# Optimization experiments

Measured on AMD Instinct MI355X. Metric: run time of the kernel, lower is better.

The kernel has to match this reference:

```python
import jax, jax.numpy as jnp
import numpy as np

B, S, D_MODEL, N_HEADS, D_K, D_V = 2, 2048, 1024, 16, 64, 64


def setup_inputs() -> dict:
    key = jax.random.key(0)
    k1, k2, k3, k4, k5, k6, k7 = jax.random.split(key, 7)
    scale = 1.0 / np.sqrt(D_MODEL)
    inputs = {
        "input_Q": jax.random.normal(k1, (B, S, D_MODEL), dtype=jnp.float32),
        "input_K": jax.random.normal(k2, (B, S, D_MODEL), dtype=jnp.float32),
        "input_V": jax.random.normal(k3, (B, S, D_MODEL), dtype=jnp.float32),
        # causal mask: True means position is masked out (matches masked_fill_)
        "attn_mask": jnp.broadcast_to(
            ~jnp.tril(jnp.ones((S, S), dtype=bool)), (B, S, S)
        ),
        "flag": 0,
        "W_Q": jax.random.normal(k4, (D_MODEL, N_HEADS * D_K), dtype=jnp.float32) * scale,
        "W_K": jax.random.normal(k5, (D_MODEL, N_HEADS * D_K), dtype=jnp.float32) * scale,
        "W_V": jax.random.normal(k6, (D_MODEL, N_HEADS * D_V), dtype=jnp.float32) * scale,
        "W_O": jax.random.normal(k7, (N_HEADS * D_V, D_MODEL), dtype=jnp.float32) * scale,
    }
    return inputs


def reference(input_Q, input_K, input_V, attn_mask, flag, W_Q, W_K, W_V, W_O):
    b = input_Q.shape[0]
    # project and split heads: [b, h, s, d]
    Q = (input_Q @ W_Q).reshape(b, -1, N_HEADS, D_K).transpose(0, 2, 1, 3)
    K = (input_K @ W_K).reshape(b, -1, N_HEADS, D_K).transpose(0, 2, 1, 3)
    V = (input_V @ W_V).reshape(b, -1, N_HEADS, D_V).transpose(0, 2, 1, 3)
    # scaled dot-product attention with additive large-negative masking
    scores = jnp.einsum("bhqd,bhkd->bhqk", Q, K) / np.sqrt(D_K).astype(np.float32)
    scores = jnp.where(attn_mask[:, None, :, :], jnp.float32(-1e9), scores)
    attn = jax.nn.softmax(scores, axis=-1)
    context = jnp.einsum("bhqk,bhkd->bhqd", attn, V)  # [b, h, s, d_v]
    context = context.transpose(0, 2, 1, 3).reshape(b, -1, N_HEADS * D_V)
    return context @ W_O
```

## Files before the change

### kernel.cpp

```cpp
#include <hip/hip_runtime.h>

#define DEVINL __device__ __forceinline__

typedef __attribute__((ext_vector_type(8))) short short8;
typedef __attribute__((ext_vector_type(4))) float floatx4;

constexpr int S_LEN = 2048;
constexpr int DM    = 1024;
constexpr int NHEAD = 16;
constexpr int DHEAD = 64;
constexpr int BATCH = 2;
constexpr int MROWS = BATCH * S_LEN;
constexpr float LOG2E = 1.44269504f;
constexpr float SM_C1 = 0.125f * LOG2E;
constexpr float SM_C2 = -24.0f * LOG2E;

DEVINL unsigned short f2bf(float x) {
  union { float f; unsigned u; } un; un.f = x;
  unsigned u = un.u;
  return (unsigned short)((u + 0x7fffu + ((u >> 16) & 1u)) >> 16);
}
DEVINL unsigned short f2bf_fast(float x) {
  union { float f; unsigned u; } un; un.f = x;
  return (unsigned short)((un.u + 0x8000u) >> 16);
}

__global__ __launch_bounds__(256) void conv3_kernel(const float* __restrict__ s0,
                                                    const float* __restrict__ s1,
                                                    const float* __restrict__ s2,
                                                    unsigned short* __restrict__ d0,
                                                    unsigned short* __restrict__ d1,
                                                    unsigned short* __restrict__ d2) {
  const float* s = blockIdx.y == 0 ? s0 : (blockIdx.y == 1 ? s1 : s2);
  unsigned short* d = blockIdx.y == 0 ? d0 : (blockIdx.y == 1 ? d1 : d2);
  int i = (blockIdx.x * 256 + threadIdx.x) * 4;
  float4 v = *(const float4*)(s + i);
  unsigned lo = (unsigned)f2bf(v.x) | ((unsigned)f2bf(v.y) << 16);
  unsigned hi = (unsigned)f2bf(v.z) | ((unsigned)f2bf(v.w) << 16);
  *(uint2*)(d + i) = make_uint2(lo, hi);
}

__global__ __launch_bounds__(256) void trans4_kernel(const float* __restrict__ W0,
                                                     const float* __restrict__ W1,
                                                     const float* __restrict__ W2,
                                                     const float* __restrict__ W3,
                                                     unsigned short* __restrict__ T0,
                                                     unsigned short* __restrict__ T1,
                                                     unsigned short* __restrict__ T2,
                                                     unsigned short* __restrict__ T3) {
  const float* W = blockIdx.z == 0 ? W0 : (blockIdx.z == 1 ? W1 : (blockIdx.z == 2 ? W2 : W3));
  unsigned short* Wt = blockIdx.z == 0 ? T0 : (blockIdx.z == 1 ? T1 : (blockIdx.z == 2 ? T2 : T3));
  __shared__ unsigned short tile[32][33];
  int t = threadIdx.x;
  int c = t & 31, r0 = t >> 5;
  int nB = blockIdx.x * 32, kB = blockIdx.y * 32;
  for (int i = 0; i < 4; ++i) {
    int r = r0 + i * 8;
    tile[r][c] = f2bf(W[(size_t)(kB + r) * DM + nB + c]);
  }
  __syncthreads();
  for (int i = 0; i < 4; ++i) {
    int r = r0 + i * 8;
    Wt[(size_t)(nB + r) * DM + kB + c] = tile[c][r];
  }
}

__global__ __launch_bounds__(256) void vtrans_kernel(const unsigned short* __restrict__ vp,
                                                     unsigned short* __restrict__ vt) {
  const int bh = blockIdx.x;
  const int st = blockIdx.y;
  const int b = bh >> 4, h = bh & 15;
  const int s0 = st * 64;
  const int tid = threadIdx.x;
  __shared__ alignas(16) unsigned short tile[64 * 72];
#pragma unroll
  for (int j = 0; j < 2; ++j) {
    int ch = j * 256 + tid;
    int r = ch >> 3, c8 = (ch & 7) * 8;
    *(uint4*)&tile[r * 72 + c8] =
        *(const uint4*)&vp[((size_t)(b * S_LEN + s0 + r)) * DM + h * DHEAD + c8];
  }
  __syncthreads();
#pragma unroll
  for (int j = 0; j < 2; ++j) {
    int ch = j * 256 + tid;
    int d = ch >> 3, s8 = (ch & 7) * 8;
    unsigned short w[8];
#pragma unroll
    for (int e = 0; e < 8; ++e) w[e] = tile[(s8 + e) * 72 + d];
    *(uint4*)&vt[((size_t)(bh * DHEAD + d)) * S_LEN + s0 + s8] = *(const uint4*)w;
  }
}

DEVINL void load_lds16(const unsigned short* g, unsigned short* l) {
  __builtin_amdgcn_global_load_lds((const __attribute__((address_space(1))) unsigned int*)g,
                                   (__attribute__((address_space(3))) unsigned int*)l,
                                   16, 0, 0);
}

template <int MODE>
DEVINL void gemm_body(const unsigned short* __restrict__ A,
                      const unsigned short* __restrict__ Bt,
                      void* __restrict__ Cout) {
  constexpr int K = 1024, N = 1024;
  __shared__ alignas(16) unsigned short As[128 * 32];
  __shared__ alignas(16) unsigned short Bs[128 * 32];
  const int tid  = threadIdx.x;
  const int wave = tid >> 6, lane = tid & 63;
  const int quad = lane >> 4, l16 = lane & 15;
  const int mBase = blockIdx.y * 128, nBase = blockIdx.x * 128;
  const int wm = (wave >> 1) * 64, wn = (wave & 1) * 64;
  const int sr = lane >> 2;
  const int sc = (lane & 3) * 8;
  floatx4 acc[4][4] = {};

  for (int k0 = 0; k0 < K; k0 += 32) {
    __syncthreads();
#pragma unroll
    for (int j = 0; j < 2; ++j) {
      int row = wave * 32 + j * 16 + sr;
      load_lds16(A  + (size_t)(mBase + row) * K + k0 + sc, As + (wave * 32 + j * 16) * 32);
      load_lds16(Bt + (size_t)(nBase + row) * K + k0 + sc, Bs + (wave * 32 + j * 16) * 32);
    }
    __syncthreads();
    short8 af[4], bfr[4];
#pragma unroll
    for (int mt = 0; mt < 4; ++mt) af[mt]  = *(const short8*)&As[(wm + mt * 16 + l16) * 32 + quad * 8];
#pragma unroll
    for (int nt = 0; nt < 4; ++nt) bfr[nt] = *(const short8*)&Bs[(wn + nt * 16 + l16) * 32 + quad * 8];
#pragma unroll
    for (int mt = 0; mt < 4; ++mt)
#pragma unroll
      for (int nt = 0; nt < 4; ++nt)
        acc[mt][nt] = __builtin_amdgcn_mfma_f32_16x16x32_bf16(af[mt], bfr[nt], acc[mt][nt], 0, 0, 0);
  }

#pragma unroll
  for (int mt = 0; mt < 4; ++mt)
#pragma unroll
    for (int nt = 0; nt < 4; ++nt)
#pragma unroll
      for (int r = 0; r < 4; ++r) {
        int m = mBase + wm + mt * 16 + quad * 4 + r;
        int n = nBase + wn + nt * 16 + l16;
        if (MODE == 0) ((unsigned short*)Cout)[(size_t)m * N + n] = f2bf(acc[mt][nt][r]);
        else           ((float*)Cout)[(size_t)m * N + n]          = acc[mt][nt][r];
      }
}

__global__ __launch_bounds__(256) void gemm_qkv(const unsigned short* __restrict__ A0,
                                                const unsigned short* __restrict__ A1,
                                                const unsigned short* __restrict__ A2,
                                                const unsigned short* __restrict__ B0,
                                                const unsigned short* __restrict__ B1,
                                                const unsigned short* __restrict__ B2,
                                                unsigned short* __restrict__ C0,
                                                unsigned short* __restrict__ C1,
                                                unsigned short* __restrict__ C2) {
  const int z = blockIdx.z;
  const unsigned short* A  = z == 0 ? A0 : (z == 1 ? A1 : A2);
  const unsigned short* Bt = z == 0 ? B0 : (z == 1 ? B1 : B2);
  unsigned short* C        = z == 0 ? C0 : (z == 1 ? C1 : C2);
  gemm_body<0>(A, Bt, C);
}

__global__ __launch_bounds__(256) void gemm_out(const unsigned short* __restrict__ A,
                                                const unsigned short* __restrict__ Bt,
                                                float* __restrict__ C) {
  gemm_body<1>(A, Bt, C);
}

__global__ __launch_bounds__(256) void attn_kernel(const unsigned short* __restrict__ Qp,
                                                   const unsigned short* __restrict__ Kp,
                                                   const unsigned short* __restrict__ Vtg,
                                                   unsigned short* __restrict__ ctx) {
  const int qt = gridDim.x - 1 - blockIdx.x;
  const int bh = blockIdx.y;
  const int b  = bh >> 4, h = bh & 15;
  const int tid = threadIdx.x;
  const int wave = tid >> 6, lane = tid & 63;
  const int quad = lane >> 4, l16 = lane & 15;
  const int Q0 = qt * 128;
  const int nT = 2 * qt + 2;

  __shared__ alignas(16) unsigned short Ks[64 * 72];
  __shared__ alignas(16) unsigned short Vs[64 * 72];
  __shared__ alignas(16) unsigned short Ps[4][32 * 72];

  const unsigned short* Kbh = Kp  + (size_t)(b * S_LEN) * DM + h * DHEAD;
  const unsigned short* Vbh = Vtg + (size_t)(bh * DHEAD) * S_LEN;

  const int sr = tid >> 3, sc8 = (tid & 7) * 8;
  const unsigned short* kptr = Kbh + (size_t)sr * DM + sc8;
  const unsigned short* vptr = Vbh + (size_t)sr * S_LEN + sc8;
  unsigned short* ksl = Ks + sr * 72 + sc8;
  unsigned short* vsl = Vs + sr * 72 + sc8;

  const int rowbase = Q0 + wave * 32;
  short8 qf[2][2];
#pragma unroll
  for (int mt = 0; mt < 2; ++mt) {
    const size_t qrow = ((size_t)(b * S_LEN + rowbase + mt * 16 + l16)) * DM + h * DHEAD;
    qf[mt][0] = *(const short8*)&Qp[qrow + quad * 8];
    qf[mt][1] = *(const short8*)&Qp[qrow + 32 + quad * 8];
  }

  floatx4 o[2][4] = {};
  float rs[2][4] = {};
  unsigned short* Pw = &Ps[wave][0];

  uint4 kr0 = *(const uint4*)kptr;
  uint4 kr1 = *(const uint4*)(kptr + (size_t)32 * DM);
  uint4 vr0 = *(const uint4*)vptr;
  uint4 vr1 = *(const uint4*)(vptr + (size_t)32 * S_LEN);

  for (int t = 0; t < nT; ++t) {
    const int kb = t * 64;
    __syncthreads();
    *(uint4*)ksl              = kr0;
    *(uint4*)(ksl + 32 * 72)  = kr1;
    *(uint4*)vsl              = vr0;
    *(uint4*)(vsl + 32 * 72)  = vr1;
    __syncthreads();

    {
      const int kbn = (t + 1 < nT) ? (t + 1) * 64 : 0;
      kr0 = *(const uint4*)(kptr + (size_t)kbn * DM);
      kr1 = *(const uint4*)(kptr + (size_t)(kbn + 32) * DM);
      vr0 = *(const uint4*)(vptr + kbn);
      vr1 = *(const uint4*)(vptr + (size_t)32 * S_LEN + kbn);
    }

    floatx4 sc[2][4];
#pragma unroll
    for (int nt = 0; nt < 4; ++nt) {
      short8 kf0 = *(const short8*)&Ks[(nt * 16 + l16) * 72 + quad * 8];
      short8 kf1 = *(const short8*)&Ks[(nt * 16 + l16) * 72 + 32 + quad * 8];
#pragma unroll
      for (int mt = 0; mt < 2; ++mt) {
        floatx4 a = {};
        a = __builtin_amdgcn_mfma_f32_16x16x32_bf16(qf[mt][0], kf0, a, 0, 0, 0);
        a = __builtin_amdgcn_mfma_f32_16x16x32_bf16(qf[mt][1], kf1, a, 0, 0, 0);
        sc[mt][nt] = a;
      }
    }

    const bool masked = (t >= nT - 2);
#pragma unroll
    for (int mt = 0; mt < 2; ++mt)
#pragma unroll
      for (int nt = 0; nt < 4; ++nt) {
        const int colg = kb + nt * 16 + l16;
#pragma unroll
        for (int r = 0; r < 4; ++r) {
          float p = __builtin_amdgcn_exp2f(fmaf(sc[mt][nt][r], SM_C1, SM_C2));
          if (masked && colg > rowbase + mt * 16 + quad * 4 + r) p = 0.f;
          rs[mt][r] += p;
          Pw[(mt * 16 + quad * 4 + r) * 72 + nt * 16 + l16] = f2bf_fast(p);
        }
      }

    short8 vf[4][2];
#pragma unroll
    for (int dt = 0; dt < 4; ++dt) {
      vf[dt][0] = *(const short8*)&Vs[(dt * 16 + l16) * 72 + quad * 8];
      vf[dt][1] = *(const short8*)&Vs[(dt * 16 + l16) * 72 + 32 + quad * 8];
    }
#pragma unroll
    for (int mt = 0; mt < 2; ++mt) {
      short8 pf0 = *(const short8*)&Pw[(mt * 16 + l16) * 72 + quad * 8];
      short8 pf1 = *(const short8*)&Pw[(mt * 16 + l16) * 72 + 32 + quad * 8];
#pragma unroll
      for (int dt = 0; dt < 4; ++dt) {
        o[mt][dt] = __builtin_amdgcn_mfma_f32_16x16x32_bf16(pf0, vf[dt][0], o[mt][dt], 0, 0, 0);
        o[mt][dt] = __builtin_amdgcn_mfma_f32_16x16x32_bf16(pf1, vf[dt][1], o[mt][dt], 0, 0, 0);
      }
    }
  }

#pragma unroll
  for (int mt = 0; mt < 2; ++mt)
#pragma unroll
    for (int r = 0; r < 4; ++r) {
      float l = rs[mt][r];
#pragma unroll
      for (int off = 1; off < 16; off <<= 1) l += __shfl_xor(l, off, 64);
      float inv = 1.0f / l;
      const size_t row = (size_t)(b * S_LEN + rowbase + mt * 16 + quad * 4 + r);
#pragma unroll
      for (int dt = 0; dt < 4; ++dt)
        ctx[row * DM + h * DHEAD + dt * 16 + l16] = f2bf(o[mt][dt][r] * inv);
    }
}

extern "C" void kernel_launch(void* const* d_in, const int* in_sizes, int n_in,
                              void* d_out, int out_size, void* d_ws, size_t ws_size,
                              hipStream_t stream) {
  const float* Xq = (const float*)d_in[0];
  const float* Xk = (const float*)d_in[1];
  const float* Xv = (const float*)d_in[2];
  const float* Wq = (const float*)d_in[5];
  const float* Wk = (const float*)d_in[6];
  const float* Wv = (const float*)d_in[7];
  const float* Wo = (const float*)d_in[8];
  float* out = (float*)d_out;

  char* ws = (char*)d_ws;
  constexpr size_t XBYTES = (size_t)MROWS * DM * 2;
  constexpr size_t WBYTES = (size_t)DM * DM * 2;
  unsigned short* xq_bf = (unsigned short*)(ws);
  unsigned short* xk_bf = (unsigned short*)(ws + XBYTES);
  unsigned short* xv_bf = (unsigned short*)(ws + 2 * XBYTES);
  unsigned short* wqt   = (unsigned short*)(ws + 3 * XBYTES);
  unsigned short* wkt   = (unsigned short*)(ws + 3 * XBYTES + WBYTES);
  unsigned short* wvt   = (unsigned short*)(ws + 3 * XBYTES + 2 * WBYTES);
  unsigned short* wot   = (unsigned short*)(ws + 3 * XBYTES + 3 * WBYTES);
  unsigned short* qp    = (unsigned short*)(ws + 3 * XBYTES + 4 * WBYTES);
  unsigned short* kp    = (unsigned short*)(ws + 4 * XBYTES + 4 * WBYTES);
  unsigned short* vp    = (unsigned short*)(ws + 5 * XBYTES + 4 * WBYTES);
  unsigned short* ctx   = xq_bf;
  unsigned short* vt    = xk_bf;

  const int nX = MROWS * DM;
  conv3_kernel<<<dim3(nX / 1024, 3), 256, 0, stream>>>(Xq, Xk, Xv, xq_bf, xk_bf, xv_bf);
  trans4_kernel<<<dim3(32, 32, 4), 256, 0, stream>>>(Wq, Wk, Wv, Wo, wqt, wkt, wvt, wot);

  gemm_qkv<<<dim3(DM / 128, MROWS / 128, 3), 256, 0, stream>>>(
      xq_bf, xk_bf, xv_bf, wqt, wkt, wvt, qp, kp, vp);

  vtrans_kernel<<<dim3(BATCH * NHEAD, S_LEN / 64), 256, 0, stream>>>(vp, vt);

  attn_kernel<<<dim3(S_LEN / 128, BATCH * NHEAD), 256, 0, stream>>>(qp, kp, vt, ctx);

  gemm_out<<<dim3(DM / 128, MROWS / 128), 256, 0, stream>>>(ctx, wot, out);
}
```

Before: 270.5 us.

## Pair short and long causal query tiles per block to balance attention work

Each attention block now processes two 64-row query tiles, one from the start and one mirrored from the end of the sequence, so every block covers the same number of key tiles (33) instead of the triangular imbalance of 128-row tiles. The K/V tiles loaded into shared memory are shared by both query tiles. The short tile's work is skipped by a branch once its causal range ends. The P scratch stride also changes from 72 to 68 to alter LDS bank mapping. The grid shrinks to 16x32 blocks. Each block holds state for two tiles and runs a uniform but longer loop.

```diff
diff --git a/kernel.cpp b/kernel.cpp
--- a/kernel.cpp
+++ b/kernel.cpp
@@ -14,6 +14,7 @@
 constexpr float LOG2E = 1.44269504f;
 constexpr float SM_C1 = 0.125f * LOG2E;
 constexpr float SM_C2 = -24.0f * LOG2E;
+constexpr int PSTR = 68;
 
 DEVINL unsigned short f2bf(float x) {
   union { float f; unsigned u; } un; un.f = x;
@@ -174,18 +175,20 @@
                                                    const unsigned short* __restrict__ Kp,
                                                    const unsigned short* __restrict__ Vtg,
                                                    unsigned short* __restrict__ ctx) {
-  const int qt = gridDim.x - 1 - blockIdx.x;
+  const int kpair = blockIdx.x;
   const int bh = blockIdx.y;
   const int b  = bh >> 4, h = bh & 15;
   const int tid = threadIdx.x;
   const int wave = tid >> 6, lane = tid & 63;
   const int quad = lane >> 4, l16 = lane & 15;
-  const int Q0 = qt * 128;
-  const int nT = 2 * qt + 2;
+  const int Q0A = kpair * 64;
+  const int Q0B = (31 - kpair) * 64;
+  const int nTA = kpair + 1;
+  const int nTB = 32 - kpair;
 
   __shared__ alignas(16) unsigned short Ks[64 * 72];
   __shared__ alignas(16) unsigned short Vs[64 * 72];
-  __shared__ alignas(16) unsigned short Ps[4][32 * 72];
+  __shared__ alignas(16) unsigned short Ps[4][32 * PSTR];
 
   const unsigned short* Kbh = Kp  + (size_t)(b * S_LEN) * DM + h * DHEAD;
   const unsigned short* Vbh = Vtg + (size_t)(bh * DHEAD) * S_LEN;
@@ -196,17 +199,23 @@
   unsigned short* ksl = Ks + sr * 72 + sc8;
   unsigned short* vsl = Vs + sr * 72 + sc8;
 
-  const int rowbase = Q0 + wave * 32;
-  short8 qf[2][2];
-#pragma unroll
-  for (int mt = 0; mt < 2; ++mt) {
-    const size_t qrow = ((size_t)(b * S_LEN + rowbase + mt * 16 + l16)) * DM + h * DHEAD;
-    qf[mt][0] = *(const short8*)&Qp[qrow + quad * 8];
-    qf[mt][1] = *(const short8*)&Qp[qrow + 32 + quad * 8];
-  }
-
-  floatx4 o[2][4] = {};
-  float rs[2][4] = {};
+  const int rowA = Q0A + wave * 16;
+  const int rowB = Q0B + wave * 16;
+
+  short8 qfA[2], qfB[2];
+  {
+    const size_t qr = ((size_t)(b * S_LEN + rowA + l16)) * DM + h * DHEAD;
+    qfA[0] = *(const short8*)&Qp[qr + quad * 8];
+    qfA[1] = *(const short8*)&Qp[qr + 32 + quad * 8];
+  }
+  {
+    const size_t qr = ((size_t)(b * S_LEN + rowB + l16)) * DM + h * DHEAD;
+    qfB[0] = *(const short8*)&Qp[qr + quad * 8];
+    qfB[1] = *(const short8*)&Qp[qr + 32 + quad * 8];
+  }
+
+  floatx4 oA[4] = {}, oB[4] = {};
+  float rsA[4] = {}, rsB[4] = {};
   unsigned short* Pw = &Ps[wave][0];
 
   uint4 kr0 = *(const uint4*)kptr;
@@ -214,51 +223,68 @@
   uint4 vr0 = *(const uint4*)vptr;
   uint4 vr1 = *(const uint4*)(vptr + (size_t)32 * S_LEN);
 
-  for (int t = 0; t < nT; ++t) {
+  for (int t = 0; t < nTB; ++t) {
     const int kb = t * 64;
     __syncthreads();
-    *(uint4*)ksl              = kr0;
-    *(uint4*)(ksl + 32 * 72)  = kr1;
-    *(uint4*)vsl              = vr0;
-    *(uint4*)(vsl + 32 * 72)  = vr1;
+    *(uint4*)ksl             = kr0;
+    *(uint4*)(ksl + 32 * 72) = kr1;
+    *(uint4*)vsl             = vr0;
+    *(uint4*)(vsl + 32 * 72) = vr1;
     __syncthreads();
 
     {
-      const int kbn = (t + 1 < nT) ? (t + 1) * 64 : 0;
+      const int kbn = (t + 1 < nTB) ? (t + 1) * 64 : 0;
       kr0 = *(const uint4*)(kptr + (size_t)kbn * DM);
       kr1 = *(const uint4*)(kptr + (size_t)(kbn + 32) * DM);
       vr0 = *(const uint4*)(vptr + kbn);
       vr1 = *(const uint4*)(vptr + (size_t)32 * S_LEN + kbn);
     }
 
-    floatx4 sc[2][4];
+    const bool aAct  = (t < nTA);
+    const bool maskA = (t == nTA - 1);
+    const bool maskB = (t == nTB - 1);
+
+    floatx4 sA[4], sB[4];
 #pragma unroll
     for (int nt = 0; nt < 4; ++nt) {
       short8 kf0 = *(const short8*)&Ks[(nt * 16 + l16) * 72 + quad * 8];
       short8 kf1 = *(const short8*)&Ks[(nt * 16 + l16) * 72 + 32 + quad * 8];
-#pragma unroll
-      for (int mt = 0; mt < 2; ++mt) {
+      if (aAct) {
         floatx4 a = {};
-        a = __builtin_amdgcn_mfma_f32_16x16x32_bf16(qf[mt][0], kf0, a, 0, 0, 0);
-        a = __builtin_amdgcn_mfma_f32_16x16x32_bf16(qf[mt][1], kf1, a, 0, 0, 0);
-        sc[mt][nt] = a;
-      }
-    }
-
-    const bool masked = (t >= nT - 2);
-#pragma unroll
-    for (int mt = 0; mt < 2; ++mt)
+        a = __builtin_amdgcn_mfma_f32_16x16x32_bf16(qfA[0], kf0, a, 0, 0, 0);
+        a = __builtin_amdgcn_mfma_f32_16x16x32_bf16(qfA[1], kf1, a, 0, 0, 0);
+        sA[nt] = a;
+      }
+      floatx4 c = {};
+      c = __builtin_amdgcn_mfma_f32_16x16x32_bf16(qfB[0], kf0, c, 0, 0, 0);
+      c = __builtin_amdgcn_mfma_f32_16x16x32_bf16(qfB[1], kf1, c, 0, 0, 0);
+      sB[nt] = c;
+    }
+
+    if (aAct) {
 #pragma unroll
       for (int nt = 0; nt < 4; ++nt) {
         const int colg = kb + nt * 16 + l16;
 #pragma unroll
         for (int r = 0; r < 4; ++r) {
-          float p = __builtin_amdgcn_exp2f(fmaf(sc[mt][nt][r], SM_C1, SM_C2));
-          if (masked && colg > rowbase + mt * 16 + quad * 4 + r) p = 0.f;
-          rs[mt][r] += p;
-          Pw[(mt * 16 + quad * 4 + r) * 72 + nt * 16 + l16] = f2bf_fast(p);
+          float p = __builtin_amdgcn_exp2f(fmaf(sA[nt][r], SM_C1, SM_C2));
+          if (maskA && colg > rowA + quad * 4 + r) p = 0.f;
+          rsA[r] += p;
+          Pw[(quad * 4 + r) * PSTR + nt * 16 + l16] = f2bf_fast(p);
         }
       }
+    }
+#pragma unroll
+    for (int nt = 0; nt < 4; ++nt) {
+      const int colg = kb + nt * 16 + l16;
+#pragma unroll
+      for (int r = 0; r < 4; ++r) {
+        float p = __builtin_amdgcn_exp2f(fmaf(sB[nt][r], SM_C1, SM_C2));
+        if (maskB && colg > rowB + quad * 4 + r) p = 0.f;
+        rsB[r] += p;
+        Pw[(16 + quad * 4 + r) * PSTR + nt * 16 + l16] = f2bf_fast(p);
+      }
+    }
 
     short8 vf[4][2];
 #pragma unroll
@@ -266,31 +292,43 @@
       vf[dt][0] = *(const short8*)&Vs[(dt * 16 + l16) * 72 + quad * 8];
       vf[dt][1] = *(const short8*)&Vs[(dt * 16 + l16) * 72 + 32 + quad * 8];
     }
-#pragma unroll
-    for (int mt = 0; mt < 2; ++mt) {
-      short8 pf0 = *(const short8*)&Pw[(mt * 16 + l16) * 72 + quad * 8];
-      short8 pf1 = *(const short8*)&Pw[(mt * 16 + l16) * 72 + 32 + quad * 8];
+    if (aAct) {
+      short8 pf0 = *(const short8*)&Pw[l16 * PSTR + quad * 8];
+      short8 pf1 = *(const short8*)&Pw[l16 * PSTR + 32 + quad * 8];
 #pragma unroll
       for (int dt = 0; dt < 4; ++dt) {
-        o[mt][dt] = __builtin_amdgcn_mfma_f32_16x16x32_bf16(pf0, vf[dt][0], o[mt][dt], 0, 0, 0);
-        o[mt][dt] = __builtin_amdgcn_mfma_f32_16x16x32_bf16(pf1, vf[dt][1], o[mt][dt], 0, 0, 0);
-      }
-    }
-  }
-
-#pragma unroll
-  for (int mt = 0; mt < 2; ++mt)
-#pragma unroll
-    for (int r = 0; r < 4; ++r) {
-      float l = rs[mt][r];
-#pragma unroll
-      for (int off = 1; off < 16; off <<= 1) l += __shfl_xor(l, off, 64);
-      float inv = 1.0f / l;
-      const size_t row = (size_t)(b * S_LEN + rowbase + mt * 16 + quad * 4 + r);
-#pragma unroll
-      for (int dt = 0; dt < 4; ++dt)
-        ctx[row * DM + h * DHEAD + dt * 16 + l16] = f2bf(o[mt][dt][r] * inv);
-    }
+        oA[dt] = __builtin_amdgcn_mfma_f32_16x16x32_bf16(pf0, vf[dt][0], oA[dt], 0, 0, 0);
+        oA[dt] = __builtin_amdgcn_mfma_f32_16x16x32_bf16(pf1, vf[dt][1], oA[dt], 0, 0, 0);
+      }
+    }
+    {
+      short8 pf0 = *(const short8*)&Pw[(16 + l16) * PSTR + quad * 8];
+      short8 pf1 = *(const short8*)&Pw[(16 + l16) * PSTR + 32 + quad * 8];
+#pragma unroll
+      for (int dt = 0; dt < 4; ++dt) {
+        oB[dt] = __builtin_amdgcn_mfma_f32_16x16x32_bf16(pf0, vf[dt][0], oB[dt], 0, 0, 0);
+        oB[dt] = __builtin_amdgcn_mfma_f32_16x16x32_bf16(pf1, vf[dt][1], oB[dt], 0, 0, 0);
+      }
+    }
+  }
+
+#pragma unroll
+  for (int r = 0; r < 4; ++r) {
+    float lA = rsA[r], lB = rsB[r];
+#pragma unroll
+    for (int off = 1; off < 16; off <<= 1) {
+      lA += __shfl_xor(lA, off, 64);
+      lB += __shfl_xor(lB, off, 64);
+    }
+    const float invA = 1.0f / lA, invB = 1.0f / lB;
+    const size_t ra = (size_t)(b * S_LEN + rowA + quad * 4 + r);
+    const size_t rb = (size_t)(b * S_LEN + rowB + quad * 4 + r);
+#pragma unroll
+    for (int dt = 0; dt < 4; ++dt) {
+      ctx[ra * DM + h * DHEAD + dt * 16 + l16] = f2bf(oA[dt][r] * invA);
+      ctx[rb * DM + h * DHEAD + dt * 16 + l16] = f2bf(oB[dt][r] * invB);
+    }
+  }
 }
 
 extern "C" void kernel_launch(void* const* d_in, const int* in_sizes, int n_in,
@@ -330,7 +368,7 @@
 
   vtrans_kernel<<<dim3(BATCH * NHEAD, S_LEN / 64), 256, 0, stream>>>(vp, vt);
 
-  attn_kernel<<<dim3(S_LEN / 128, BATCH * NHEAD), 256, 0, stream>>>(qp, kp, vt, ctx);
+  attn_kernel<<<dim3(16, BATCH * NHEAD), 256, 0, stream>>>(qp, kp, vt, ctx);
 
   gemm_out<<<dim3(DM / 128, MROWS / 128), 256, 0, stream>>>(ctx, wot, out);
 }
```

Result: faster. 264.7 us (-2.1%).
